# Kernel optimization log

Measured on AMD Instinct MI355X. Metric: run time of the kernel, lower is better.

Reference implementation:

```python
import jax, jax.numpy as jnp
import numpy as np

E = 1024      # hidden_size
H = 16        # num_attention_heads
HD = E // H   # head_dim
EPS = 1e-5


def _mw_linear(x, Wt, bt, Wi, bi, split):
    # multiway linear: text weights on tokens [:split], image weights on [split:]
    xt = x[:, :split] @ Wt.T + bt
    xi = x[:, split:] @ Wi.T + bi
    return jnp.concatenate([xt, xi], axis=1)


def _ln(x, g, b):
    mu = jnp.mean(x, axis=-1, keepdims=True)
    var = jnp.mean(jnp.square(x - mu), axis=-1, keepdims=True)
    return (x - mu) * jax.lax.rsqrt(var + EPS) * g + b


def _mw_ln(x, gt, bt, gi, bi, split):
    return jnp.concatenate([_ln(x[:, :split], gt, bt), _ln(x[:, split:], gi, bi)], axis=1)


def setup_inputs() -> dict:
    key = jax.random.key(0)
    ks = jax.random.split(key, 24)
    B, T = 8, 1024
    d = {
        'query': jax.random.normal(ks[0], (B, T, E), jnp.float32),
        'key': jax.random.normal(ks[1], (B, T, E), jnp.float32),
        'value': jax.random.normal(ks[2], (B, T, E), jnp.float32),
        'attention_mask': jax.random.normal(ks[3], (T, T), jnp.float32) * 0.02,
    }
    i = 4
    for name in ['q', 'k', 'v', 'o']:
        d[f'W{name}_t'] = jax.random.normal(ks[i], (E, E), jnp.float32) * 0.02; i += 1
        d[f'b{name}_t'] = jnp.zeros((E,), jnp.float32)
        d[f'W{name}_i'] = jax.random.normal(ks[i], (E, E), jnp.float32) * 0.02; i += 1
        d[f'b{name}_i'] = jnp.zeros((E,), jnp.float32)
    d['ln_g_t'] = jnp.ones((E,), jnp.float32)
    d['ln_b_t'] = jnp.zeros((E,), jnp.float32)
    d['ln_g_i'] = jnp.ones((E,), jnp.float32)
    d['ln_b_i'] = jnp.zeros((E,), jnp.float32)
    d['split_position'] = 64
    return d


def reference(query, key, value, attention_mask,
              Wq_t, bq_t, Wq_i, bq_i,
              Wk_t, bk_t, Wk_i, bk_i,
              Wv_t, bv_t, Wv_i, bv_i,
              Wo_t, bo_t, Wo_i, bo_i,
              ln_g_t, ln_b_t, ln_g_i, ln_b_i,
              split_position):
    B, T, _ = query.shape
    S = key.shape[1]
    scaling = HD ** -0.5
    q = _mw_linear(query, Wq_t, bq_t, Wq_i, bq_i, split_position) * scaling
    k = _mw_linear(key, Wk_t, bk_t, Wk_i, bk_i, split_position)
    v = _mw_linear(value, Wv_t, bv_t, Wv_i, bv_i, split_position)
    q = q.reshape(B, T, H, HD)
    k = k.reshape(B, S, H, HD)
    v = v.reshape(B, S, H, HD)
    # [B, H, T, S] attention logits
    attn_weights = jnp.einsum('bthd,bshd->bhts', q, k)
    attn_weights = jnp.nan_to_num(attn_weights) + attention_mask[None, None]
    probs = jax.nn.softmax(attn_weights.astype(jnp.float32), axis=-1).astype(attn_weights.dtype)
    attn = jnp.einsum('bhts,bshd->bthd', probs, v).reshape(B, T, E)
    attn = _mw_ln(attn, ln_g_t, ln_b_t, ln_g_i, ln_b_i, split_position)
    attn = _mw_linear(attn, Wo_t, bo_t, Wo_i, bo_i, split_position)
    return attn
```

## Files before the change

kernel.cpp:

```cpp
#include <hip/hip_runtime.h>

#define E_DIM 1024
#define HEADS 16
#define HD 64
#define LOG2E 1.44269504088896340736f

typedef unsigned short ushort_t;
typedef __attribute__((ext_vector_type(8))) short bf16x8;
typedef __attribute__((ext_vector_type(4))) float floatx4;
typedef __attribute__((ext_vector_type(4))) float f32x4;
typedef __attribute__((ext_vector_type(16))) float floatx16;

__device__ inline unsigned int pack2bf(float a, float b) {
    unsigned int ua = __builtin_bit_cast(unsigned int, a);
    unsigned int ub = __builtin_bit_cast(unsigned int, b);
    ua = (ua + 0x8000u) >> 16;
    ub = (ub + 0x8000u) & 0xFFFF0000u;
    return ua | ub;
}
__device__ inline unsigned short f2bf(float a) {
    return (unsigned short)((__builtin_bit_cast(unsigned int, a) + 0x8000u) >> 16);
}
__device__ inline float bf2f(unsigned int s) {
    return __builtin_bit_cast(float, s << 16);
}

__device__ __forceinline__ void load_lds16(const void* g, void* l) {
    __builtin_amdgcn_global_load_lds(
        (const __attribute__((address_space(1))) unsigned int*)g,
        (__attribute__((address_space(3))) unsigned int*)l, 16, 0, 0);
}

__global__ __launch_bounds__(256) void cvt_inputs(
    const float* s0, const float* s1, const float* s2,
    ushort_t* d0, ushort_t* d1, ushort_t* d2)
{
    const float* __restrict__ src = (blockIdx.y == 0) ? s0 : (blockIdx.y == 1) ? s1 : s2;
    ushort_t* __restrict__ dst = (blockIdx.y == 0) ? d0 : (blockIdx.y == 1) ? d1 : d2;
    size_t i = ((size_t)blockIdx.x * 256 + threadIdx.x) * 8;
    float4 a = *(const float4*)&src[i];
    float4 b = *(const float4*)&src[i + 4];
    uint4 o;
    o.x = pack2bf(a.x, a.y); o.y = pack2bf(a.z, a.w);
    o.z = pack2bf(b.x, b.y); o.w = pack2bf(b.z, b.w);
    *(uint4*)&dst[i] = o;
}

__global__ __launch_bounds__(256) void cvt_weights(
    const float* w0, const float* w1, const float* w2, const float* w3,
    const float* w4, const float* w5, const float* w6, const float* w7,
    ushort_t* __restrict__ out)
{
    const float* srcs[8] = {w0, w1, w2, w3, w4, w5, w6, w7};
    const float* __restrict__ src = srcs[blockIdx.y];
    ushort_t* __restrict__ dst = out + (size_t)blockIdx.y * E_DIM * E_DIM;
    size_t i = ((size_t)blockIdx.x * 256 + threadIdx.x) * 8;
    float4 a = *(const float4*)&src[i];
    float4 b = *(const float4*)&src[i + 4];
    uint4 o;
    o.x = pack2bf(a.x, a.y); o.y = pack2bf(a.z, a.w);
    o.z = pack2bf(b.x, b.y); o.w = pack2bf(b.z, b.w);
    *(uint4*)&dst[i] = o;
}

__global__ __launch_bounds__(256) void mask_pack(
    const float* __restrict__ m, float* __restrict__ mp, int T_)
{
    int gid = blockIdx.x * 256 + threadIdx.x;
    int t  = gid >> 8;
    int s4 = (gid & 255) * 4;
    float4 v = *(const float4*)&m[(size_t)t * T_ + s4];
    int qt = t >> 5, q32 = t & 31;
    int it = s4 >> 6, s6 = s4 & 63;
    int j = s6 >> 5, up = (s6 >> 3) & 3, hi = (s6 >> 2) & 1;
    int L = j * 4 + up, lane = q32 + 32 * hi;
    size_t o = (((size_t)(qt * 16 + it) * 8 + L) * 64 + lane) * 4;
    float4 ov;
    ov.x = v.x * LOG2E - 16.0f; ov.y = v.y * LOG2E - 16.0f;
    ov.z = v.z * LOG2E - 16.0f; ov.w = v.w * LOG2E - 16.0f;
    *(float4*)&mp[o] = ov;
}

template<bool OUT_BF16>
__device__ __forceinline__ void gemm_core(
    const ushort_t* __restrict__ x, const ushort_t* __restrict__ W,
    const float* __restrict__ bias, void* __restrict__ outv,
    int m0, int n0, int split, int kind, float scale, int T_)
{
    __shared__ __align__(16) ushort_t As[128 * 32];
    __shared__ __align__(16) ushort_t Bs[128 * 32];

    const int tid  = threadIdx.x;
    const int lane = tid & 63;
    const int wv   = tid >> 6;
    const int rw   = (wv >> 1) * 64;
    const int cw   = (wv & 1) * 64;
    const int am   = lane & 15;
    const int aq   = lane >> 4;

    const int grow = wv * 32 + (lane >> 2);
    const int gcol = (lane & 3) * 8;

    floatx4 acc[4][4];
    #pragma unroll
    for (int i = 0; i < 4; ++i)
        #pragma unroll
        for (int j = 0; j < 4; ++j)
            acc[i][j] = (floatx4){0.f, 0.f, 0.f, 0.f};

    for (int k0 = 0; k0 < E_DIM; k0 += 32) {
        load_lds16(&x[(size_t)(m0 + grow) * E_DIM + k0 + gcol],      &As[(wv * 32) * 32]);
        load_lds16(&x[(size_t)(m0 + grow + 16) * E_DIM + k0 + gcol], &As[(wv * 32 + 16) * 32]);
        load_lds16(&W[(size_t)(n0 + grow) * E_DIM + k0 + gcol],      &Bs[(wv * 32) * 32]);
        load_lds16(&W[(size_t)(n0 + grow + 16) * E_DIM + k0 + gcol], &Bs[(wv * 32 + 16) * 32]);
        __syncthreads();

        bf16x8 af[4], bfv[4];
        #pragma unroll
        for (int i = 0; i < 4; ++i)
            af[i] = *(const bf16x8*)&As[(rw + i * 16 + am) * 32 + aq * 8];
        #pragma unroll
        for (int j = 0; j < 4; ++j)
            bfv[j] = *(const bf16x8*)&Bs[(cw + j * 16 + am) * 32 + aq * 8];

        #pragma unroll
        for (int i = 0; i < 4; ++i)
            #pragma unroll
            for (int j = 0; j < 4; ++j)
                acc[i][j] = __builtin_amdgcn_mfma_f32_16x16x32_bf16(af[i], bfv[j], acc[i][j], 0, 0, 0);
        __syncthreads();
    }

    const int cq = lane >> 4;
    const int cm = lane & 15;
    #pragma unroll
    for (int j = 0; j < 4; ++j) {
        int n = n0 + cw + j * 16 + cm;
        float bv = bias[n];
        #pragma unroll
        for (int i = 0; i < 4; ++i) {
            int mbase = m0 + rw + i * 16 + cq * 4;
            #pragma unroll
            for (int r = 0; r < 4; ++r) {
                int m = mbase + r;
                int t = m % T_;
                if (((t < split) ? 0 : 1) != kind) continue;
                float val = (acc[i][j][r] + bv) * scale;
                if (OUT_BF16) ((ushort_t*)outv)[(size_t)m * E_DIM + n] = f2bf(val);
                else          ((float*)outv)[(size_t)m * E_DIM + n] = val;
            }
        }
    }
}

__global__ __launch_bounds__(256) void gemm_qkv(
    const ushort_t* __restrict__ xq, const ushort_t* __restrict__ xk,
    const ushort_t* __restrict__ xv, const ushort_t* __restrict__ wall,
    const float* bq_t, const float* bq_i, const float* bk_t, const float* bk_i,
    const float* bv_t, const float* bv_i,
    ushort_t* oq, ushort_t* ok, ushort_t* ov,
    const int* __restrict__ split_ptr, int T_)
{
    const int split = *split_ptr;
    const int z = blockIdx.z;
    const int op = z >> 1;
    const int kind = z & 1;
    const int m0 = blockIdx.y * 128;
    const int n0 = blockIdx.x * 128;
    const int t0 = m0 % T_;

    if (kind == 0) { if (t0 >= split) return; }
    else           { if (t0 + 128 <= split) return; }

    const ushort_t* x = (op == 0) ? xq : (op == 1) ? xk : xv;
    ushort_t* outp    = (op == 0) ? oq : (op == 1) ? ok : ov;
    const ushort_t* W = wall + (size_t)z * E_DIM * E_DIM;
    const float* bias = (op == 0) ? (kind ? bq_i : bq_t)
                      : (op == 1) ? (kind ? bk_i : bk_t)
                                  : (kind ? bv_i : bv_t);
    float scale = (op == 0) ? 0.125f * LOG2E : 1.0f;

    gemm_core<true>(x, W, bias, outp, m0, n0, split, kind, scale, T_);
}

__global__ __launch_bounds__(256) void gemm_o(
    const ushort_t* __restrict__ x, const ushort_t* __restrict__ Wt,
    const float* bt, const ushort_t* __restrict__ Wi, const float* bi,
    float* __restrict__ outp, const int* __restrict__ split_ptr, int T_)
{
    const int split = *split_ptr;
    const int kind = blockIdx.z;
    const int m0 = blockIdx.y * 128;
    const int n0 = blockIdx.x * 128;
    const int t0 = m0 % T_;

    if (kind == 0) { if (t0 >= split) return; }
    else           { if (t0 + 128 <= split) return; }

    gemm_core<false>(x, kind ? Wi : Wt, kind ? bi : bt, outp, m0, n0, split, kind, 1.0f, T_);
}

__global__ __launch_bounds__(256) void attn_mfma32(
    const ushort_t* __restrict__ q, const ushort_t* __restrict__ k,
    const ushort_t* __restrict__ v, const float* __restrict__ maskP,
    ushort_t* __restrict__ outp, int T_)
{
    const int tid  = threadIdx.x;
    const int lane = tid & 63;
    const int wv   = tid >> 6;
    const int b    = blockIdx.x;
    const int h    = blockIdx.y;
    const int r0   = blockIdx.z * 128;

    const int q32 = lane & 31;
    const int hi  = lane >> 5;

    __shared__ __align__(16) ushort_t Ks[64 * 72];
    __shared__ __align__(16) ushort_t VT[64 * 72];

    const int qrow = r0 + wv * 32 + q32;
    const int qt16 = ((r0 >> 5) + wv) * 16;

    bf16x8 aqf[4];
    #pragma unroll
    for (int dc = 0; dc < 4; ++dc)
        aqf[dc] = *(const bf16x8*)&q[((size_t)(b * T_ + qrow)) * E_DIM + h * HD + dc * 16 + hi * 8];

    floatx16 oa[2];
    #pragma unroll
    for (int n = 0; n < 2; ++n)
        #pragma unroll
        for (int i = 0; i < 16; ++i) oa[n][i] = 0.f;
    float lsum = 0.f;

    const int kr = tid >> 2;
    const int kc = (tid & 3) * 16;
    const int vr = (tid >> 4) * 4;
    const int vc = (tid & 15) * 4;

    uint4 kreg[2];
    uint2 vreg[4];

    kreg[0] = *(const uint4*)&k[((size_t)(b * T_ + kr)) * E_DIM + h * HD + kc];
    kreg[1] = *(const uint4*)&k[((size_t)(b * T_ + kr)) * E_DIM + h * HD + kc + 8];
    #pragma unroll
    for (int i = 0; i < 4; ++i)
        vreg[i] = *(const uint2*)&v[((size_t)(b * T_ + vr + i)) * E_DIM + h * HD + vc];

    *(uint4*)&Ks[kr * 72 + kc]     = kreg[0];
    *(uint4*)&Ks[kr * 72 + kc + 8] = kreg[1];
    {
        const ushort_t* vp = (const ushort_t*)vreg;
        #pragma unroll
        for (int t = 0; t < 4; ++t) {
            uint2 w;
            w.x = (unsigned int)vp[0 * 4 + t] | ((unsigned int)vp[1 * 4 + t] << 16);
            w.y = (unsigned int)vp[2 * 4 + t] | ((unsigned int)vp[3 * 4 + t] << 16);
            *(uint2*)&VT[(vc + t) * 72 + vr] = w;
        }
    }
    __syncthreads();

    const int NT = T_ / 64;
    #pragma unroll 1
    for (int it = 0; it < NT; ++it) {
        const int s0 = it * 64;

        if (it + 1 < NT) {
            const int sn = s0 + 64;
            kreg[0] = *(const uint4*)&k[((size_t)(b * T_ + sn + kr)) * E_DIM + h * HD + kc];
            kreg[1] = *(const uint4*)&k[((size_t)(b * T_ + sn + kr)) * E_DIM + h * HD + kc + 8];
            #pragma unroll
            for (int i = 0; i < 4; ++i)
                vreg[i] = *(const uint2*)&v[((size_t)(b * T_ + sn + vr + i)) * E_DIM + h * HD + vc];
        }

        f32x4 mk[8];
        {
            const float* mp = maskP + ((size_t)(qt16 + it) << 11) + (lane << 2);
            #pragma unroll
            for (int L = 0; L < 8; ++L)
                mk[L] = *(const f32x4*)&mp[L << 8];
        }

        floatx16 sa[2];
        #pragma unroll
        for (int j = 0; j < 2; ++j)
            #pragma unroll
            for (int i = 0; i < 16; ++i) sa[j][i] = 0.f;
        __builtin_amdgcn_s_setprio(1);
        #pragma unroll
        for (int j = 0; j < 2; ++j)
            #pragma unroll
            for (int dc = 0; dc < 4; ++dc) {
                bf16x8 kf = *(const bf16x8*)&Ks[(32 * j + q32) * 72 + dc * 16 + hi * 8];
                sa[j] = __builtin_amdgcn_mfma_f32_32x32x16_bf16(kf, aqf[dc], sa[j], 0, 0, 0);
            }
        __builtin_amdgcn_s_setprio(0);

        float lp0 = 0.f, lp1 = 0.f, lp2 = 0.f, lp3 = 0.f;
        #pragma unroll
        for (int j = 0; j < 2; ++j)
            #pragma unroll
            for (int i = 0; i < 16; ++i) {
                float e = exp2f(sa[j][i] + mk[(j << 2) | (i >> 2)][i & 3]);
                sa[j][i] = e;
                if ((i & 3) == 0) lp0 += e;
                else if ((i & 3) == 1) lp1 += e;
                else if ((i & 3) == 2) lp2 += e;
                else lp3 += e;
            }
        lsum += (lp0 + lp1) + (lp2 + lp3);

        unsigned int W[2][8], X[2][8];
        #pragma unroll
        for (int j = 0; j < 2; ++j)
            #pragma unroll
            for (int u = 0; u < 8; ++u)
                W[j][u] = pack2bf(sa[j][2 * u], sa[j][2 * u + 1]);
        #pragma unroll
        for (int j = 0; j < 2; ++j)
            #pragma unroll
            for (int u = 0; u < 8; ++u)
                X[j][u] = (unsigned int)__shfl_xor((int)W[j][u], 32, 64);

        __builtin_amdgcn_s_setprio(1);
        #pragma unroll
        for (int s = 0; s < 4; ++s) {
            const int j = s >> 1;
            const int hh = (s & 1) * 4;
            union { unsigned int u[4]; bf16x8 v8; } pf;
            pf.u[0] = hi ? X[j][hh + 2] : W[j][hh + 0];
            pf.u[1] = hi ? X[j][hh + 3] : W[j][hh + 1];
            pf.u[2] = hi ? W[j][hh + 2] : X[j][hh + 0];
            pf.u[3] = hi ? W[j][hh + 3] : X[j][hh + 1];
            #pragma unroll
            for (int n = 0; n < 2; ++n) {
                bf16x8 vf = *(const bf16x8*)&VT[(n * 32 + q32) * 72 + s * 16 + hi * 8];
                oa[n] = __builtin_amdgcn_mfma_f32_32x32x16_bf16(pf.v8, vf, oa[n], 0, 0, 0);
            }
        }
        __builtin_amdgcn_s_setprio(0);

        if (it + 1 < NT) {
            __syncthreads();
            *(uint4*)&Ks[kr * 72 + kc]     = kreg[0];
            *(uint4*)&Ks[kr * 72 + kc + 8] = kreg[1];
            const ushort_t* vp = (const ushort_t*)vreg;
            #pragma unroll
            for (int t = 0; t < 4; ++t) {
                uint2 w;
                w.x = (unsigned int)vp[0 * 4 + t] | ((unsigned int)vp[1 * 4 + t] << 16);
                w.y = (unsigned int)vp[2 * 4 + t] | ((unsigned int)vp[3 * 4 + t] << 16);
                *(uint2*)&VT[(vc + t) * 72 + vr] = w;
            }
            __syncthreads();
        }
    }

    lsum += __shfl_xor(lsum, 32, 64);
    float inv = 1.0f / lsum;
    #pragma unroll
    for (int i = 0; i < 16; ++i) {
        int qi = (i & 3) + 8 * (i >> 2) + 4 * hi;
        float vi = __shfl(inv, qi + (lane & 32), 64);
        size_t orow = ((size_t)(b * T_ + r0 + wv * 32 + qi)) * E_DIM + h * HD;
        outp[orow + q32]      = f2bf(oa[0][i] * vi);
        outp[orow + 32 + q32] = f2bf(oa[1][i] * vi);
    }
}

__global__ __launch_bounds__(256) void mw_ln_bf16(
    const ushort_t* __restrict__ x,
    const float* __restrict__ gt, const float* __restrict__ bt,
    const float* __restrict__ gi, const float* __restrict__ bi,
    ushort_t* __restrict__ out,
    const int* __restrict__ split_ptr, int T_)
{
    const int split = *split_ptr;
    const int row = blockIdx.x;
    const int t = row % T_;
    const float* __restrict__ g  = (t < split) ? gt : gi;
    const float* __restrict__ bb = (t < split) ? bt : bi;

    const int tid = threadIdx.x;
    const int lane = tid & 63;
    const int wid = tid >> 6;

    __shared__ float red[8];

    uint2 xv = *(const uint2*)&x[(size_t)row * E_DIM + tid * 4];
    float f0 = bf2f(xv.x & 0xffffu), f1 = bf2f(xv.x >> 16);
    float f2 = bf2f(xv.y & 0xffffu), f3 = bf2f(xv.y >> 16);
    float s = f0 + f1 + f2 + f3;
    #pragma unroll
    for (int off = 1; off < 64; off <<= 1) s += __shfl_xor(s, off, 64);
    if (lane == 0) red[wid] = s;
    __syncthreads();
    float mu = (red[0] + red[1] + red[2] + red[3]) * (1.0f / E_DIM);

    float d0 = f0 - mu, d1 = f1 - mu, d2 = f2 - mu, d3 = f3 - mu;
    float s2 = d0*d0 + d1*d1 + d2*d2 + d3*d3;
    #pragma unroll
    for (int off = 1; off < 64; off <<= 1) s2 += __shfl_xor(s2, off, 64);
    if (lane == 0) red[4 + wid] = s2;
    __syncthreads();
    float var = (red[4] + red[5] + red[6] + red[7]) * (1.0f / E_DIM);
    float rstd = rsqrtf(var + 1e-5f);

    float4 gv = *(const float4*)&g[tid * 4];
    float4 bv = *(const float4*)&bb[tid * 4];
    uint2 ov;
    ov.x = pack2bf(d0 * rstd * gv.x + bv.x, d1 * rstd * gv.y + bv.y);
    ov.y = pack2bf(d2 * rstd * gv.z + bv.z, d3 * rstd * gv.w + bv.w);
    *(uint2*)&out[(size_t)row * E_DIM + tid * 4] = ov;
}

extern "C" void kernel_launch(void* const* d_in, const int* in_sizes, int n_in,
                              void* d_out, int out_size, void* d_ws, size_t ws_size,
                              hipStream_t stream) {
    const float* query = (const float*)d_in[0];
    const float* key   = (const float*)d_in[1];
    const float* value = (const float*)d_in[2];
    const float* mask  = (const float*)d_in[3];
    const float* Wq_t = (const float*)d_in[4];  const float* bq_t = (const float*)d_in[5];
    const float* Wq_i = (const float*)d_in[6];  const float* bq_i = (const float*)d_in[7];
    const float* Wk_t = (const float*)d_in[8];  const float* bk_t = (const float*)d_in[9];
    const float* Wk_i = (const float*)d_in[10]; const float* bk_i = (const float*)d_in[11];
    const float* Wv_t = (const float*)d_in[12]; const float* bv_t = (const float*)d_in[13];
    const float* Wv_i = (const float*)d_in[14]; const float* bv_i = (const float*)d_in[15];
    const float* Wo_t = (const float*)d_in[16]; const float* bo_t = (const float*)d_in[17];
    const float* Wo_i = (const float*)d_in[18]; const float* bo_i = (const float*)d_in[19];
    const float* ln_g_t = (const float*)d_in[20]; const float* ln_b_t = (const float*)d_in[21];
    const float* ln_g_i = (const float*)d_in[22]; const float* ln_b_i = (const float*)d_in[23];
    const int* split = (const int*)d_in[24];

    float* out = (float*)d_out;

    const int BT = in_sizes[0] / E_DIM;
    const int T_ = 1024;
    const int B  = BT / T_;

    ushort_t* ws = (ushort_t*)d_ws;
    const size_t nx = (size_t)BT * E_DIM;
    const size_t nw = (size_t)E_DIM * E_DIM;
    ushort_t* xq_bf = ws;
    ushort_t* xk_bf = ws + nx;
    ushort_t* xv_bf = ws + 2 * nx;
    ushort_t* k_bf  = ws + 3 * nx;
    ushort_t* v_bf  = ws + 4 * nx;
    ushort_t* w_bf  = ws + 5 * nx;
    ushort_t* q_bf  = (ushort_t*)d_out;
    float* maskP    = (float*)xk_bf;

    dim3 blk(256);
    const int cvt_blocks = (int)(nx / 2048);
    const int wcvt_blocks = (int)(nw / 2048);

    cvt_weights<<<dim3(wcvt_blocks, 8), blk, 0, stream>>>(
        Wq_t, Wq_i, Wk_t, Wk_i, Wv_t, Wv_i, Wo_t, Wo_i, w_bf);
    cvt_inputs<<<dim3(cvt_blocks, 3), blk, 0, stream>>>(
        query, key, value, xq_bf, xk_bf, xv_bf);

    gemm_qkv<<<dim3(E_DIM / 128, BT / 128, 6), blk, 0, stream>>>(
        xq_bf, xk_bf, xv_bf, w_bf,
        bq_t, bq_i, bk_t, bk_i, bv_t, bv_i,
        q_bf, k_bf, v_bf, split, T_);

    mask_pack<<<dim3(T_ * T_ / 4 / 256), blk, 0, stream>>>(mask, maskP, T_);

    attn_mfma32<<<dim3(B, HEADS, T_ / 128), blk, 0, stream>>>(
        q_bf, k_bf, v_bf, maskP, q_bf, T_);

    mw_ln_bf16<<<dim3(BT), blk, 0, stream>>>(
        q_bf, ln_g_t, ln_b_t, ln_g_i, ln_b_i, xq_bf, split, T_);

    gemm_o<<<dim3(E_DIM / 128, BT / 128, 2), blk, 0, stream>>>(
        xq_bf, w_bf + 6 * nw, bo_t, w_bf + 7 * nw, bo_i, out, split, T_);
}
```

Baseline: 472.6 us.

## Double-buffer GEMM LDS tiles and remap grid to pack text-split blocks

Makes the GEMM K-loop double-buffered in LDS: the next 32-wide K slice is prefetched while MFMAs run on the current one, which leaves one barrier per iteration. It also swaps the grid axes so blockIdx.x indexes M tiles. For the text (kind 0) weights, blocks are packed so that only the needed batch×ceil(split/128) M tiles have real work, and the excess blocks exit early. The cost is twice the LDS per block, which may lower occupancy. With a single barrier, it relies on the end-of-iteration sync to keep a buffer from being overwritten before all reads finish.

```diff
diff --git a/kernel.cpp b/kernel.cpp
--- a/kernel.cpp
+++ b/kernel.cpp
@@ -87,8 +87,8 @@
     const float* __restrict__ bias, void* __restrict__ outv,
     int m0, int n0, int split, int kind, float scale, int T_)
 {
-    __shared__ __align__(16) ushort_t As[128 * 32];
-    __shared__ __align__(16) ushort_t Bs[128 * 32];
+    __shared__ __align__(16) ushort_t As[2][128 * 32];
+    __shared__ __align__(16) ushort_t Bs[2][128 * 32];
 
     const int tid  = threadIdx.x;
     const int lane = tid & 63;
@@ -108,26 +108,37 @@
         for (int j = 0; j < 4; ++j)
             acc[i][j] = (floatx4){0.f, 0.f, 0.f, 0.f};
 
+    load_lds16(&x[(size_t)(m0 + grow) * E_DIM + gcol],      &As[0][(wv * 32) * 32]);
+    load_lds16(&x[(size_t)(m0 + grow + 16) * E_DIM + gcol], &As[0][(wv * 32 + 16) * 32]);
+    load_lds16(&W[(size_t)(n0 + grow) * E_DIM + gcol],      &Bs[0][(wv * 32) * 32]);
+    load_lds16(&W[(size_t)(n0 + grow + 16) * E_DIM + gcol], &Bs[0][(wv * 32 + 16) * 32]);
+    __syncthreads();
+
     for (int k0 = 0; k0 < E_DIM; k0 += 32) {
-        load_lds16(&x[(size_t)(m0 + grow) * E_DIM + k0 + gcol],      &As[(wv * 32) * 32]);
-        load_lds16(&x[(size_t)(m0 + grow + 16) * E_DIM + k0 + gcol], &As[(wv * 32 + 16) * 32]);
-        load_lds16(&W[(size_t)(n0 + grow) * E_DIM + k0 + gcol],      &Bs[(wv * 32) * 32]);
-        load_lds16(&W[(size_t)(n0 + grow + 16) * E_DIM + k0 + gcol], &Bs[(wv * 32 + 16) * 32]);
-        __syncthreads();
+        const int cur = (k0 >> 5) & 1;
+        if (k0 + 32 < E_DIM) {
+            const int nxt = cur ^ 1;
+            const int kn  = k0 + 32;
+            load_lds16(&x[(size_t)(m0 + grow) * E_DIM + kn + gcol],      &As[nxt][(wv * 32) * 32]);
+            load_lds16(&x[(size_t)(m0 + grow + 16) * E_DIM + kn + gcol], &As[nxt][(wv * 32 + 16) * 32]);
+            load_lds16(&W[(size_t)(n0 + grow) * E_DIM + kn + gcol],      &Bs[nxt][(wv * 32) * 32]);
+            load_lds16(&W[(size_t)(n0 + grow + 16) * E_DIM + kn + gcol], &Bs[nxt][(wv * 32 + 16) * 32]);
+        }
 
         bf16x8 af[4], bfv[4];
         #pragma unroll
         for (int i = 0; i < 4; ++i)
-            af[i] = *(const bf16x8*)&As[(rw + i * 16 + am) * 32 + aq * 8];
+            af[i] = *(const bf16x8*)&As[cur][(rw + i * 16 + am) * 32 + aq * 8];
         #pragma unroll
         for (int j = 0; j < 4; ++j)
-            bfv[j] = *(const bf16x8*)&Bs[(cw + j * 16 + am) * 32 + aq * 8];
+            bfv[j] = *(const bf16x8*)&Bs[cur][(cw + j * 16 + am) * 32 + aq * 8];
 
         #pragma unroll
         for (int i = 0; i < 4; ++i)
             #pragma unroll
             for (int j = 0; j < 4; ++j)
                 acc[i][j] = __builtin_amdgcn_mfma_f32_16x16x32_bf16(af[i], bfv[j], acc[i][j], 0, 0, 0);
+
         __syncthreads();
     }
 
@@ -153,6 +164,21 @@
     }
 }
 
+__device__ __forceinline__ int gemm_pick_m0(int kind, int split, int T_, bool& ok)
+{
+    ok = true;
+    if (kind == 0) {
+        const int nq = (split + 127) >> 7;
+        const int Bb = (int)(gridDim.x * 128) / T_;
+        if ((int)blockIdx.x >= Bb * nq) { ok = false; return 0; }
+        const int batch = blockIdx.x / nq, tq = blockIdx.x % nq;
+        return batch * T_ + tq * 128;
+    }
+    const int m0 = blockIdx.x * 128;
+    if ((m0 % T_) + 128 <= split) { ok = false; return 0; }
+    return m0;
+}
+
 __global__ __launch_bounds__(256) void gemm_qkv(
     const ushort_t* __restrict__ xq, const ushort_t* __restrict__ xk,
     const ushort_t* __restrict__ xv, const ushort_t* __restrict__ wall,
@@ -165,12 +191,11 @@
     const int z = blockIdx.z;
     const int op = z >> 1;
     const int kind = z & 1;
-    const int m0 = blockIdx.y * 128;
-    const int n0 = blockIdx.x * 128;
-    const int t0 = m0 % T_;
-
-    if (kind == 0) { if (t0 >= split) return; }
-    else           { if (t0 + 128 <= split) return; }
+    const int n0 = blockIdx.y * 128;
+
+    bool ok2;
+    const int m0 = gemm_pick_m0(kind, split, T_, ok2);
+    if (!ok2) return;
 
     const ushort_t* x = (op == 0) ? xq : (op == 1) ? xk : xv;
     ushort_t* outp    = (op == 0) ? oq : (op == 1) ? ok : ov;
@@ -190,12 +215,11 @@
 {
     const int split = *split_ptr;
     const int kind = blockIdx.z;
-    const int m0 = blockIdx.y * 128;
-    const int n0 = blockIdx.x * 128;
-    const int t0 = m0 % T_;
-
-    if (kind == 0) { if (t0 >= split) return; }
-    else           { if (t0 + 128 <= split) return; }
+    const int n0 = blockIdx.y * 128;
+
+    bool ok2;
+    const int m0 = gemm_pick_m0(kind, split, T_, ok2);
+    if (!ok2) return;
 
     gemm_core<false>(x, kind ? Wi : Wt, kind ? bi : bt, outp, m0, n0, split, kind, 1.0f, T_);
 }
@@ -462,7 +486,7 @@
     cvt_inputs<<<dim3(cvt_blocks, 3), blk, 0, stream>>>(
         query, key, value, xq_bf, xk_bf, xv_bf);
 
-    gemm_qkv<<<dim3(E_DIM / 128, BT / 128, 6), blk, 0, stream>>>(
+    gemm_qkv<<<dim3(BT / 128, E_DIM / 128, 6), blk, 0, stream>>>(
         xq_bf, xk_bf, xv_bf, w_bf,
         bq_t, bq_i, bk_t, bk_i, bv_t, bv_i,
         q_bf, k_bf, v_bf, split, T_);
@@ -475,6 +499,6 @@
     mw_ln_bf16<<<dim3(BT), blk, 0, stream>>>(
         q_bf, ln_g_t, ln_b_t, ln_g_i, ln_b_i, xq_bf, split, T_);
 
-    gemm_o<<<dim3(E_DIM / 128, BT / 128, 2), blk, 0, stream>>>(
+    gemm_o<<<dim3(BT / 128, E_DIM / 128, 2), blk, 0, stream>>>(
         xq_bf, w_bf + 6 * nw, bo_t, w_bf + 7 * nw, bo_i, out, split, T_);
 }
```

After: 477.6 us. About the same (+1.0%).
